# Optimization experiments

Measured on AMD Instinct MI355X. Metric: run time of the kernel, lower is better.

Reference implementation:

```python
import jax, jax.numpy as jnp
import numpy as np

OUT = (7, 7, 7)      # output_size (D_out, H_out, W_out)
SCALE = 1.0          # spatial_scale


def setup_inputs() -> dict:
    key = jax.random.key(0)
    k1, k2 = jax.random.split(key)
    B, C, D, H, W = 2, 256, 64, 64, 64
    N = 512
    features = jax.random.normal(k1, (B, C, D, H, W), dtype=jnp.float32)
    p = jax.random.uniform(k2, (B, N, 6), dtype=jnp.float32) * 63.0
    lo = jnp.minimum(p[..., :3], p[..., 3:])
    hi = jnp.maximum(p[..., :3], p[..., 3:])
    proposals = jnp.concatenate([lo, hi], axis=-1)  # (B, N, 6) valid boxes
    return {"features": features, "proposals": proposals}


def _trilinear(vol, gz, gy, gx):
    # vol: (C, D, H, W); gz/gy/gx: (Do, Ho, Wo) voxel-space coords.
    # grid_sample(mode='bilinear', padding_mode='zeros', align_corners=True)
    C, D, H, W = vol.shape
    z0f, y0f, x0f = jnp.floor(gz), jnp.floor(gy), jnp.floor(gx)
    wz, wy, wx = gz - z0f, gy - y0f, gx - x0f
    z0, y0, x0 = z0f.astype(jnp.int32), y0f.astype(jnp.int32), x0f.astype(jnp.int32)

    def gather(zi, yi, xi):
        valid = (zi >= 0) & (zi < D) & (yi >= 0) & (yi < H) & (xi >= 0) & (xi < W)
        v = vol[:, jnp.clip(zi, 0, D - 1), jnp.clip(yi, 0, H - 1), jnp.clip(xi, 0, W - 1)]
        return v * valid.astype(vol.dtype)[None]  # (C, Do, Ho, Wo)

    out = jnp.zeros((C,) + gz.shape, dtype=vol.dtype)
    for dz in (0, 1):
        for dy in (0, 1):
            for dx in (0, 1):
                w = ((wz if dz else 1.0 - wz)
                     * (wy if dy else 1.0 - wy)
                     * (wx if dx else 1.0 - wx))
                out = out + gather(z0 + dz, y0 + dy, x0 + dx) * w[None]
    return out


def reference(features, proposals):
    # features: (B, C, D, H, W); proposals: (B, N, 6) [x1,y1,z1,x2,y2,z2]
    B, C, D, H, W = features.shape
    Do, Ho, Wo = OUT

    def one_roi(vol, prop):
        p = prop * SCALE
        x1, y1, z1, x2, y2, z2 = p[0], p[1], p[2], p[3], p[4], p[5]
        zc = jnp.linspace(z1, z2, Do)
        yc = jnp.linspace(y1, y2, Ho)
        xc = jnp.linspace(x1, x2, Wo)
        gz, gy, gx = jnp.meshgrid(zc, yc, xc, indexing='ij')  # (Do,Ho,Wo)
        return _trilinear(vol, gz, gy, gx)  # (C, Do, Ho, Wo)

    per_batch = jax.vmap(lambda vol, props: jax.vmap(lambda p: one_roi(vol, p))(props))
    out = per_batch(features, proposals)  # (B, N, C, Do, Ho, Wo)
    return out.reshape(B * proposals.shape[1], C, Do, Ho, Wo)
```

## Files before the change

kernel.cpp:

```cpp
#include <hip/hip_runtime.h>


#define B_     2
#define C_     256
#define N_     512
#define NENT   (N_ * 7)
#define PITCH  68
#define PLANE  (64 * PITCH)
#define THREADS 1024

__device__ __forceinline__ float gcoord(float lo, float hi, int i) {
    return lo + (hi - lo) * (1.0f / 6.0f) * (float)i;
}

__global__ __launch_bounds__(256) void bucket_kernel(
    const float* __restrict__ props, int* __restrict__ ws)
{
    int b = blockIdx.x;
    __shared__ int counts[63];
    __shared__ int starts[64];
    __shared__ int cursors[63];
    int tid = threadIdx.x;
    if (tid < 63) counts[tid] = 0;
    __syncthreads();
    for (int e = tid; e < NENT; e += 256) {
        int n = e / 7, iz = e - n * 7;
        const float* pr = props + (size_t)(b * N_ + n) * 6;
        float gz = gcoord(pr[2], pr[5], iz);
        int z0 = min(max((int)gz, 0), 62);
        atomicAdd(&counts[z0], 1);
    }
    __syncthreads();
    if (tid == 0) {
        int s = 0;
        for (int k = 0; k < 63; ++k) { starts[k] = s; s += counts[k]; }
        starts[63] = s;
    }
    __syncthreads();
    if (tid < 63) cursors[tid] = starts[tid];
    __syncthreads();
    for (int e = tid; e < NENT; e += 256) {
        int n = e / 7, iz = e - n * 7;
        const float* pr = props + (size_t)(b * N_ + n) * 6;
        float gz = gcoord(pr[2], pr[5], iz);
        int z0 = min(max((int)gz, 0), 62);
        int pos = atomicAdd(&cursors[z0], 1);
        ws[128 + b * NENT + pos] = (n << 3) | iz;
    }
    if (tid < 64) ws[b * 64 + tid] = starts[tid];
}

__global__ __launch_bounds__(THREADS, 8) void roialign3d_slice_kernel(
    const float* __restrict__ feat,
    const float* __restrict__ props,
    const int* __restrict__ ws,
    float* __restrict__ out)
{
    __shared__ __align__(16) float planes[3 * PLANE];
    __shared__ float ldsProps[N_ * 6];
    __shared__ int ldsStarts[64];

    int s = blockIdx.x;
    int b = s >> 8;
    int c = s & 255;
    const float* vol = feat + (size_t)s * (64 * 64 * 64);
    int tid  = threadIdx.x;
    int wid  = tid >> 6;
    int lane = tid & 63;

    for (int i = tid; i < N_ * 6; i += THREADS)
        ldsProps[i] = props[(size_t)b * (N_ * 6) + i];
    if (tid < 64) ldsStarts[tid] = ws[b * 64 + tid];
    int sy_ = tid >> 4, sx_ = (tid & 15) << 2;
    {
        float4 v0 = *(const float4*)(vol + (tid << 2));
        float4 v1 = *(const float4*)(vol + 4096 + (tid << 2));
        *(float4*)&planes[0 * PLANE + sy_ * PITCH + sx_] = v0;
        *(float4*)&planes[1 * PLANE + sy_ * PITCH + sx_] = v1;
    }
    __syncthreads();

    int iy_l = lane / 7;
    int ix_l = lane - iy_l * 7;
    const int* ents = ws + 128 + b * NENT;

    for (int z = 0; z < 63; ++z) {
        int slotA = z % 3;
        int slotB = (z + 1) % 3;
        int slotC = (z + 2) % 3;
        bool doStage = (z < 62);
        float4 stg;
        if (doStage)
            stg = *(const float4*)(vol + (size_t)(z + 2) * 4096 + (tid << 2));

        int base = ldsStarts[z];
        int cnt  = ldsStarts[z + 1] - base;
        for (int e = wid; e < cnt; e += 16) {
            int ent = ents[base + e];
            int n = ent >> 3, iz = ent & 7;
            const float* pr = &ldsProps[n * 6];
            float x1p = pr[0], y1p = pr[1], z1p = pr[2];
            float x2p = pr[3], y2p = pr[4], z2p = pr[5];
            if (lane < 49) {
                float gx = gcoord(x1p, x2p, ix_l);
                float gy = gcoord(y1p, y2p, iy_l);
                float gz = gcoord(z1p, z2p, iz);
                int x0 = (int)gx, y0 = (int)gy;
                float wx = gx - (float)x0;
                float wy = gy - (float)y0;
                float wz = fminf(fmaxf(gz - (float)z, 0.0f), 1.0f);
                int a00 = slotA * PLANE + y0 * PITCH + x0;
                int a01 = a00 + PITCH;
                int a10 = slotB * PLANE + y0 * PITCH + x0;
                int a11 = a10 + PITCH;
                float v000 = planes[a00], v001 = planes[a00 + 1];
                float v010 = planes[a01], v011 = planes[a01 + 1];
                float v100 = planes[a10], v101 = planes[a10 + 1];
                float v110 = planes[a11], v111 = planes[a11 + 1];
                float c00 = v000 + (v001 - v000) * wx;
                float c01 = v010 + (v011 - v010) * wx;
                float c10 = v100 + (v101 - v100) * wx;
                float c11 = v110 + (v111 - v110) * wx;
                float d0 = c00 + (c01 - c00) * wy;
                float d1 = c10 + (c11 - c10) * wy;
                float r  = d0 + (d1 - d0) * wz;
                out[((size_t)(b * N_ + n) * C_ + c) * 343 + iz * 49 + lane] = r;
            }
        }
        if (doStage)
            *(float4*)&planes[slotC * PLANE + sy_ * PITCH + sx_] = stg;
        __syncthreads();
    }
}

extern "C" void kernel_launch(void* const* d_in, const int* in_sizes, int n_in,
                              void* d_out, int out_size, void* d_ws, size_t ws_size,
                              hipStream_t stream) {
    const float* feat  = (const float*)d_in[0];
    const float* props = (const float*)d_in[1];
    float* out = (float*)d_out;
    int* ws = (int*)d_ws;

    bucket_kernel<<<2, 256, 0, stream>>>(props, ws);
    roialign3d_slice_kernel<<<B_ * C_, THREADS, 0, stream>>>(feat, props, ws, out);
}
```

Baseline: 309.3 us.

## Precompute per-entry sample records and deepen plane prefetch to four slots

The bucket kernel now writes a 32-byte record per (roi, z-slice) entry holding the x/y origin and step, the z weight and the precomputed output offset. The slice kernel reads these records through float4 loads and software-prefetches the next record, which removes the per-entry LDS proposal table and the gcoord arithmetic. The plane ring grows from three to four slots so each global plane load is issued one iteration earlier, and the launch-bounds occupancy hint is dropped. A direct-gather fallback kernel is added for when the workspace is too small, at the cost of more LDS and extra record traffic.

```diff
diff --git a/kernel.cpp b/kernel.cpp
--- a/kernel.cpp
+++ b/kernel.cpp
@@ -1,20 +1,22 @@
 #include <hip/hip_runtime.h>
 
 
-#define B_     2
-#define C_     256
-#define N_     512
-#define NENT   (N_ * 7)
-#define PITCH  68
-#define PLANE  (64 * PITCH)
+#define B_      2
+#define C_      256
+#define N_      512
+#define NENT    (N_ * 7)
+#define PITCH   68
+#define PLANE   (64 * PITCH)
 #define THREADS 1024
+#define REC_F_BASE 128
+#define WS_NEEDED ((size_t)REC_F_BASE * 4 + (size_t)B_ * NENT * 8 * 4)
 
 __device__ __forceinline__ float gcoord(float lo, float hi, int i) {
     return lo + (hi - lo) * (1.0f / 6.0f) * (float)i;
 }
 
 __global__ __launch_bounds__(256) void bucket_kernel(
-    const float* __restrict__ props, int* __restrict__ ws)
+    const float* __restrict__ props, int* __restrict__ wsi, float* __restrict__ wsf)
 {
     int b = blockIdx.x;
     __shared__ int counts[63];
@@ -42,94 +44,144 @@
     for (int e = tid; e < NENT; e += 256) {
         int n = e / 7, iz = e - n * 7;
         const float* pr = props + (size_t)(b * N_ + n) * 6;
-        float gz = gcoord(pr[2], pr[5], iz);
+        float x1p = pr[0], y1p = pr[1], z1p = pr[2];
+        float x2p = pr[3], y2p = pr[4], z2p = pr[5];
+        float gz = gcoord(z1p, z2p, iz);
         int z0 = min(max((int)gz, 0), 62);
+        float wz = gz - (float)z0;
         int pos = atomicAdd(&cursors[z0], 1);
-        ws[128 + b * NENT + pos] = (n << 3) | iz;
-    }
-    if (tid < 64) ws[b * 64 + tid] = starts[tid];
-}
-
-__global__ __launch_bounds__(THREADS, 8) void roialign3d_slice_kernel(
+        int off = (b * N_ + n) * (C_ * 343) + iz * 49;
+        float* r = wsf + REC_F_BASE + (size_t)(b * NENT + pos) * 8;
+        r[0] = x1p; r[1] = (x2p - x1p) * (1.0f / 6.0f);
+        r[2] = y1p; r[3] = (y2p - y1p) * (1.0f / 6.0f);
+        r[4] = wz;  r[5] = __int_as_float(off);
+        r[6] = 0.0f; r[7] = 0.0f;
+    }
+    if (tid < 64) wsi[b * 64 + tid] = starts[tid];
+}
+
+__global__ __launch_bounds__(THREADS) void roialign3d_slice_kernel(
     const float* __restrict__ feat,
-    const float* __restrict__ props,
-    const int* __restrict__ ws,
+    const int* __restrict__ wsi,
+    const float* __restrict__ wsf,
     float* __restrict__ out)
 {
-    __shared__ __align__(16) float planes[3 * PLANE];
-    __shared__ float ldsProps[N_ * 6];
+    __shared__ __align__(16) float planes[4 * PLANE];
     __shared__ int ldsStarts[64];
 
     int s = blockIdx.x;
     int b = s >> 8;
     int c = s & 255;
     const float* vol = feat + (size_t)s * (64 * 64 * 64);
-    int tid  = threadIdx.x;
-    int wid  = tid >> 6;
-    int lane = tid & 63;
-
-    for (int i = tid; i < N_ * 6; i += THREADS)
-        ldsProps[i] = props[(size_t)b * (N_ * 6) + i];
-    if (tid < 64) ldsStarts[tid] = ws[b * 64 + tid];
-    int sy_ = tid >> 4, sx_ = (tid & 15) << 2;
-    {
-        float4 v0 = *(const float4*)(vol + (tid << 2));
-        float4 v1 = *(const float4*)(vol + 4096 + (tid << 2));
-        *(float4*)&planes[0 * PLANE + sy_ * PITCH + sx_] = v0;
-        *(float4*)&planes[1 * PLANE + sy_ * PITCH + sx_] = v1;
-    }
-    __syncthreads();
-
-    int iy_l = lane / 7;
-    int ix_l = lane - iy_l * 7;
-    const int* ents = ws + 128 + b * NENT;
+    int tid = threadIdx.x, wid = tid >> 6, lane = tid & 63;
+
+    if (tid < 64) ldsStarts[tid] = wsi[b * 64 + tid];
+    int soff = (tid >> 4) * PITCH + ((tid & 15) << 2);
+
+    float4 v0 = *(const float4*)(vol + (tid << 2));
+    float4 v1 = *(const float4*)(vol + 4096 + (tid << 2));
+    *(float4*)&planes[0 * PLANE + soff] = v0;
+    *(float4*)&planes[1 * PLANE + soff] = v1;
+    float4 stgA = *(const float4*)(vol + 2 * 4096 + (tid << 2));
+    __syncthreads();
+
+    int iy0 = lane / 7;
+    float fx = (float)(lane - iy0 * 7);
+    float fy = (float)min(iy0, 6);
+    float* outp = out + (size_t)c * 343;
+    const float4* recs = (const float4*)(wsf + REC_F_BASE);
+    const int rbase = b * NENT;
 
     for (int z = 0; z < 63; ++z) {
-        int slotA = z % 3;
-        int slotB = (z + 1) % 3;
-        int slotC = (z + 2) % 3;
-        bool doStage = (z < 62);
-        float4 stg;
-        if (doStage)
-            stg = *(const float4*)(vol + (size_t)(z + 2) * 4096 + (tid << 2));
+        int aA = (z & 3) * PLANE;
+        int aB = ((z + 1) & 3) * PLANE;
+        int aW = ((z + 2) & 3) * PLANE;
+        float4 stgB;
+        if (z <= 60)
+            stgB = *(const float4*)(vol + (size_t)(z + 3) * 4096 + (tid << 2));
 
         int base = ldsStarts[z];
         int cnt  = ldsStarts[z + 1] - base;
-        for (int e = wid; e < cnt; e += 16) {
-            int ent = ents[base + e];
-            int n = ent >> 3, iz = ent & 7;
-            const float* pr = &ldsProps[n * 6];
-            float x1p = pr[0], y1p = pr[1], z1p = pr[2];
-            float x2p = pr[3], y2p = pr[4], z2p = pr[5];
+        int e = wid;
+        float4 rA, rB;
+        if (e < cnt) {
+            rA = recs[(rbase + base + e) * 2];
+            rB = recs[(rbase + base + e) * 2 + 1];
+        }
+        while (e < cnt) {
+            int e2 = e + 16;
+            float4 nA, nB;
+            if (e2 < cnt) {
+                nA = recs[(rbase + base + e2) * 2];
+                nB = recs[(rbase + base + e2) * 2 + 1];
+            }
             if (lane < 49) {
-                float gx = gcoord(x1p, x2p, ix_l);
-                float gy = gcoord(y1p, y2p, iy_l);
-                float gz = gcoord(z1p, z2p, iz);
+                float gx = fmaf(rA.y, fx, rA.x);
+                float gy = fmaf(rA.w, fy, rA.z);
                 int x0 = (int)gx, y0 = (int)gy;
                 float wx = gx - (float)x0;
                 float wy = gy - (float)y0;
-                float wz = fminf(fmaxf(gz - (float)z, 0.0f), 1.0f);
-                int a00 = slotA * PLANE + y0 * PITCH + x0;
-                int a01 = a00 + PITCH;
-                int a10 = slotB * PLANE + y0 * PITCH + x0;
-                int a11 = a10 + PITCH;
-                float v000 = planes[a00], v001 = planes[a00 + 1];
-                float v010 = planes[a01], v011 = planes[a01 + 1];
-                float v100 = planes[a10], v101 = planes[a10 + 1];
-                float v110 = planes[a11], v111 = planes[a11 + 1];
+                float wz = rB.x;
+                int a = y0 * PITCH + x0;
+                const float* L0 = &planes[aA + a];
+                const float* L1 = &planes[aB + a];
+                float v000 = L0[0], v001 = L0[1];
+                float v010 = L0[PITCH], v011 = L0[PITCH + 1];
+                float v100 = L1[0], v101 = L1[1];
+                float v110 = L1[PITCH], v111 = L1[PITCH + 1];
                 float c00 = v000 + (v001 - v000) * wx;
                 float c01 = v010 + (v011 - v010) * wx;
                 float c10 = v100 + (v101 - v100) * wx;
                 float c11 = v110 + (v111 - v110) * wx;
                 float d0 = c00 + (c01 - c00) * wy;
                 float d1 = c10 + (c11 - c10) * wy;
-                float r  = d0 + (d1 - d0) * wz;
-                out[((size_t)(b * N_ + n) * C_ + c) * 343 + iz * 49 + lane] = r;
+                outp[__float_as_int(rB.y) + lane] = d0 + (d1 - d0) * wz;
             }
+            e = e2; rA = nA; rB = nB;
         }
-        if (doStage)
-            *(float4*)&planes[slotC * PLANE + sy_ * PITCH + sx_] = stg;
+        if (z <= 61)
+            *(float4*)&planes[aW + soff] = stgA;
         __syncthreads();
+        stgA = stgB;
+    }
+}
+
+__global__ __launch_bounds__(128) void roialign3d_fallback(
+    const float* __restrict__ feat, const float* __restrict__ props,
+    float* __restrict__ out)
+{
+    int bid = blockIdx.x;
+    int xcd = bid & 7;
+    int j   = bid >> 3;
+    int s   = xcd + ((j >> 9) << 3);
+    int n   = j & 511;
+    int b   = s >> 8;
+    int c   = s & 255;
+    const float* prop = props + ((size_t)(b * N_ + n)) * 6;
+    float x1p = prop[0], y1p = prop[1], z1p = prop[2];
+    float x2p = prop[3], y2p = prop[4], z2p = prop[5];
+    float sx = (x2p - x1p) * (1.0f / 6.0f);
+    float sy = (y2p - y1p) * (1.0f / 6.0f);
+    float sz = (z2p - z1p) * (1.0f / 6.0f);
+    const float* vol = feat + (size_t)s * (64 * 64 * 64);
+    float* o = out + ((size_t)(b * N_ + n) * C_ + c) * 343;
+    for (int p = threadIdx.x; p < 343; p += 128) {
+        int iz = p / 49, r = p - iz * 49, iy = r / 7, ix = r - iy * 7;
+        float gx = x1p + sx * ix, gy = y1p + sy * iy, gz = z1p + sz * iz;
+        int x0 = (int)gx, y0 = (int)gy, z0 = (int)gz;
+        float wx = gx - x0, wy = gy - y0, wz = gz - z0;
+        int x1 = min(x0 + 1, 63), y1 = min(y0 + 1, 63), z1 = min(z0 + 1, 63);
+        const float* p00 = vol + ((z0 * 64 + y0) << 6);
+        const float* p01 = vol + ((z0 * 64 + y1) << 6);
+        const float* p10 = vol + ((z1 * 64 + y0) << 6);
+        const float* p11 = vol + ((z1 * 64 + y1) << 6);
+        float c00 = p00[x0] + (p00[x1] - p00[x0]) * wx;
+        float c01 = p01[x0] + (p01[x1] - p01[x0]) * wx;
+        float c10 = p10[x0] + (p10[x1] - p10[x0]) * wx;
+        float c11 = p11[x0] + (p11[x1] - p11[x0]) * wx;
+        float d0 = c00 + (c01 - c00) * wy;
+        float d1 = c10 + (c11 - c10) * wy;
+        o[p] = d0 + (d1 - d0) * wz;
     }
 }
 
@@ -139,8 +191,13 @@
     const float* feat  = (const float*)d_in[0];
     const float* props = (const float*)d_in[1];
     float* out = (float*)d_out;
-    int* ws = (int*)d_ws;
-
-    bucket_kernel<<<2, 256, 0, stream>>>(props, ws);
-    roialign3d_slice_kernel<<<B_ * C_, THREADS, 0, stream>>>(feat, props, ws, out);
-}
+
+    if (ws_size < WS_NEEDED) {
+        roialign3d_fallback<<<B_ * C_ * N_, 128, 0, stream>>>(feat, props, out);
+        return;
+    }
+    int*   wsi = (int*)d_ws;
+    float* wsf = (float*)d_ws;
+    bucket_kernel<<<B_, 256, 0, stream>>>(props, wsi, wsf);
+    roialign3d_slice_kernel<<<B_ * C_, THREADS, 0, stream>>>(feat, wsi, wsf, out);
+}
```

Result: slower. 335.1 us (+8.4%).
